# Performance work log

Hardware: AMD Instinct MI355X
Metric: run time of the kernel (lower is better)

Reference implementation:

```python
import jax, jax.numpy as jnp
import numpy as np

DIM = 2048
H = 16
KV_RANK = 512
NOPE = 128
ROPE_D = 64
VD = 128
QK = NOPE + ROPE_D  # 192
SCALE = QK ** -0.5
B, S = 2, 2048
EPS = 1e-5


def _rope(x, start_pos):
    # x: (b, s, h, d) or (b, s, d); rotate along last dim, positions along axis 1
    s = x.shape[1]
    d = x.shape[-1]
    half = d // 2
    inv_freq = 1.0 / (10000.0 ** (jnp.arange(half, dtype=jnp.float32) * (2.0 / d)))
    pos = jnp.arange(start_pos, start_pos + s, dtype=jnp.float32)
    ang = pos[:, None] * inv_freq[None, :]  # (s, half)
    cos, sin = jnp.cos(ang), jnp.sin(ang)
    if x.ndim == 4:
        cos, sin = cos[None, :, None, :], sin[None, :, None, :]
    else:
        cos, sin = cos[None, :, :], sin[None, :, :]
    x1, x2 = x[..., :half], x[..., half:]
    return jnp.concatenate([x1 * cos - x2 * sin, x2 * cos + x1 * sin], axis=-1).astype(x.dtype)


def _layernorm(x, w, b):
    mu = jnp.mean(x, axis=-1, keepdims=True)
    var = jnp.mean(jnp.square(x - mu), axis=-1, keepdims=True)
    return (x - mu) * jax.lax.rsqrt(var + EPS) * w + b


def setup_inputs() -> dict:
    key = jax.random.key(0)
    ks = jax.random.split(key, 6)
    std = 0.02
    x = jax.random.normal(ks[0], (B, S, DIM), dtype=jnp.float32)
    wq = jax.random.normal(ks[1], (H * QK, DIM), dtype=jnp.float32) * std
    wkv_a = jax.random.normal(ks[2], (KV_RANK + ROPE_D, DIM), dtype=jnp.float32) * std
    wkv_b = jax.random.normal(ks[3], (H * (NOPE + VD), KV_RANK), dtype=jnp.float32) * std
    wo = jax.random.normal(ks[4], (DIM, H * VD), dtype=jnp.float32) * std
    kv_norm_w = jnp.ones((KV_RANK,), dtype=jnp.float32)
    kv_norm_b = jnp.zeros((KV_RANK,), dtype=jnp.float32)
    return {"x": x, "wq": wq, "wkv_a": wkv_a, "kv_norm_w": kv_norm_w,
            "kv_norm_b": kv_norm_b, "wkv_b": wkv_b, "wo": wo, "start_pos": 0}


def reference(x, wq, wkv_a, kv_norm_w, kv_norm_b, wkv_b, wo, start_pos):
    b, s, _ = x.shape
    # query projection: (b,s,H,QK)
    q = (x @ wq.T).reshape(b, s, H, QK)
    q_nope, q_pe = q[..., :NOPE], q[..., NOPE:]
    q_pe = _rope(q_pe, start_pos)
    # compressed kv + rope key
    kv_all = x @ wkv_a.T                      # (b,s,KV_RANK+ROPE_D)
    kv, k_pe = kv_all[..., :KV_RANK], kv_all[..., KV_RANK:]
    k_pe = _rope(k_pe, start_pos)             # (b,s,ROPE_D)
    kvn = _layernorm(kv, kv_norm_w, kv_norm_b)  # (b,s,KV_RANK)
    # absorb path: expand compressed kv through per-head wkv_b blocks
    w = wkv_b.reshape(H, NOPE + VD, KV_RANK)
    k_nope = jnp.einsum('btc,hdc->bthd', kvn, w[:, :NOPE])   # (b,t,H,NOPE)
    v = jnp.einsum('btc,hdc->bthd', kvn, w[:, NOPE:])        # (b,t,H,VD)
    q_full = jnp.concatenate([q_nope, q_pe], axis=-1)        # (b,s,H,QK)
    k_full = jnp.concatenate(
        [k_nope, jnp.broadcast_to(k_pe[:, :, None, :], (b, s, H, ROPE_D))], axis=-1)
    scores = jnp.einsum('bshd,bthd->bhst', q_full, k_full) * SCALE
    causal = jnp.tril(jnp.ones((s, s), dtype=bool))
    scores = jnp.where(causal[None, None], scores, jnp.float32(-1e30))
    attn = jax.nn.softmax(scores, axis=-1)
    out = jnp.einsum('bhst,bthd->bshd', attn, v).reshape(b, s, H * VD)
    return out @ wo.T
```

## Files before the change

kernel.cpp:

```cpp
#include <hip/hip_runtime.h>
#include <hip/hip_bf16.h>
#include <math.h>

typedef __bf16 bf16_t;
typedef __bf16 bf16x2 __attribute__((ext_vector_type(2)));
typedef __bf16 bf16x4 __attribute__((ext_vector_type(4)));
typedef __bf16 bf16x8 __attribute__((ext_vector_type(8)));
typedef float f32x4 __attribute__((ext_vector_type(4)));

#define SEQ 2048
#define MLA_SCALE 0.07216878364870322f
#define LN_EPS 1e-5f

__device__ __forceinline__ void gload_lds16(const bf16_t* g, bf16_t* l) {
    __builtin_amdgcn_global_load_lds(
        (const __attribute__((address_space(1))) uint32_t*)(const void*)g,
        (__attribute__((address_space(3))) uint32_t*)(void*)l, 16, 0, 0);
}

__global__ __launch_bounds__(256)
void cvt_f32_bf16(const float* __restrict__ in, bf16_t* __restrict__ out, int n4) {
    for (int i = blockIdx.x * 256 + threadIdx.x; i < n4; i += gridDim.x * 256) {
        float4 v = ((const float4*)in)[i];
        bf16x4 p = { (bf16_t)v.x, (bf16_t)v.y, (bf16_t)v.z, (bf16_t)v.w };
        ((bf16x4*)out)[i] = p;
    }
}

#define G256_PHASE(TAU, KS, MH, HTO, MAT, WAITV)                               \
{                                                                              \
    const int slot_ = (2 * (TAU) + (KS)) & 3;                                  \
    bf16x8 af_[4];                                                             \
    {                                                                          \
        const bf16_t* ab_ = As + slot_ * 8192 +                                \
                            (wm2 * 128 + (MH) * 64 + lr) * 32 + rdcol;         \
        _Pragma("unroll")                                                      \
        for (int f = 0; f < 4; ++f) af_[f] = *(const bf16x8*)(ab_ + f * 512);  \
    }                                                                          \
    if ((MH) == 0) {                                                           \
        const bf16_t* bb_ = Bs + slot_ * 8192 + (wn2 * 64 + lr) * 32 + rdcol;  \
        _Pragma("unroll")                                                      \
        for (int f = 0; f < 4; ++f) bq[f] = *(const bf16x8*)(bb_ + f * 512);   \
    }                                                                          \
    if ((MAT) == 0) stageA(2 * T + 3 + (HTO)); else stageB(2 * T + 3 + (HTO)); \
    __builtin_amdgcn_s_barrier();                                              \
    asm volatile("" ::: "memory");                                             \
    __builtin_amdgcn_s_setprio(1);                                             \
    _Pragma("unroll")                                                          \
    for (int f = 0; f < 4; ++f)                                                \
        _Pragma("unroll")                                                      \
        for (int n = 0; n < 4; ++n)                                            \
            acc[(MH) * 4 + f][n] = __builtin_amdgcn_mfma_f32_16x16x32_bf16(    \
                af_[f], bq[n], acc[(MH) * 4 + f][n], 0, 0, 0);                 \
    __builtin_amdgcn_s_setprio(0);                                             \
    asm volatile("" ::: "memory");                                             \
    if (WAITV) asm volatile("s_waitcnt vmcnt(8)" ::: "memory");                \
    __builtin_amdgcn_s_barrier();                                              \
}

template<int MODE>
__global__ __launch_bounds__(512, 2)
void gemm256(const bf16_t* __restrict__ A, const bf16_t* __restrict__ B,
             float* __restrict__ C, bf16_t* __restrict__ out0,
             bf16_t* __restrict__ out1, int N, int K) {
    __shared__ __attribute__((aligned(16))) bf16_t As[32768];
    __shared__ __attribute__((aligned(16))) bf16_t Bs[32768];
    __shared__ __attribute__((aligned(16))) bf16_t Ds[8192];

    const int tid = threadIdx.x;
    const int lane = tid & 63, w = tid >> 6;
    const int lr = lane & 15, kh = lane >> 4;
    const int wm2 = w >> 2, wn2 = w & 3;
    const int bm = blockIdx.y, bn = blockIdx.x;
    const int NT = K >> 6;

    const int rdcol = 8 * (kh ^ ((lr >> 1) & 3));
    const int strow = (w << 5) + (lane >> 2);
    const int scol = 8 * ((lane & 3) ^ ((lane >> 3) & 3));

    f32x4 acc[8][4];
    #pragma unroll
    for (int i = 0; i < 8; ++i)
        #pragma unroll
        for (int j = 0; j < 4; ++j) acc[i][j] = 0.0f;

    auto stageA = [&](int ht) {
        int hs = (ht < 2 * NT) ? ht : (2 * NT - 1);
        int tau = hs >> 1, kap = hs & 1;
        const bf16_t* g = A + (size_t)(bm * 256 + strow) * K + tau * 64 + kap * 32 + scol;
        bf16_t* l = (ht < 2 * NT) ? (As + (ht & 3) * 8192 + w * 1024) : (Ds + w * 1024);
        gload_lds16(g, l);
        gload_lds16(g + (size_t)16 * K, l + 512);
    };
    auto stageB = [&](int ht) {
        int hs = (ht < 2 * NT) ? ht : (2 * NT - 1);
        int tau = hs >> 1, kap = hs & 1;
        const bf16_t* g = B + (size_t)(bn * 256 + strow) * K + tau * 64 + kap * 32 + scol;
        bf16_t* l = (ht < 2 * NT) ? (Bs + (ht & 3) * 8192 + w * 1024) : (Ds + w * 1024);
        gload_lds16(g, l);
        gload_lds16(g + (size_t)16 * K, l + 512);
    };

    stageA(0); stageB(0); stageA(1); stageB(1); stageA(2); stageB(2);
    asm volatile("s_waitcnt vmcnt(8)" ::: "memory");
    __builtin_amdgcn_s_barrier();

    for (int it = 0; it < (NT >> 1); ++it) {
        const int T = 2 * it;
        bf16x8 bq[4];
        G256_PHASE(T,     0, 0, 0, 0, 0)
        G256_PHASE(T,     0, 1, 0, 1, 1)
        G256_PHASE(T,     1, 0, 1, 0, 0)
        G256_PHASE(T,     1, 1, 1, 1, 1)
        G256_PHASE(T + 1, 0, 0, 2, 0, 0)
        G256_PHASE(T + 1, 0, 1, 2, 1, 1)
        G256_PHASE(T + 1, 1, 0, 3, 0, 0)
        G256_PHASE(T + 1, 1, 1, 3, 1, 1)
    }

    const int rg = kh * 4;
    if (MODE == 0) {
        #pragma unroll
        for (int mf = 0; mf < 8; ++mf)
            #pragma unroll
            for (int nf = 0; nf < 4; ++nf) {
                size_t row0 = (size_t)(bm * 256 + wm2 * 128 + mf * 16 + rg);
                int col = bn * 256 + wn2 * 64 + nf * 16 + lr;
                #pragma unroll
                for (int rr = 0; rr < 4; ++rr)
                    C[(row0 + rr) * N + col] = acc[mf][nf][rr];
            }
    } else if (MODE == 1) {
        const int h = bn;
        #pragma unroll
        for (int mf = 0; mf < 8; ++mf)
            #pragma unroll
            for (int nf = 0; nf < 4; ++nf) {
                int d = wn2 * 64 + nf * 16 + lr;
                int trow = bm * 256 + wm2 * 128 + mf * 16 + rg;
                int b = trow >> 11, t = trow & 2047;
                if (d < 128) {
                    bf16_t* p = out0 + ((size_t)(b * 16 + h) * SEQ + t) * 192 + d;
                    #pragma unroll
                    for (int rr = 0; rr < 4; ++rr)
                        p[rr * 192] = (bf16_t)acc[mf][nf][rr];
                } else {
                    bf16x4 pv = { (bf16_t)acc[mf][nf][0], (bf16_t)acc[mf][nf][1],
                                  (bf16_t)acc[mf][nf][2], (bf16_t)acc[mf][nf][3] };
                    *(bf16x4*)(out1 + ((size_t)(b * 16 + h) * 128 + (d - 128)) * SEQ + t) = pv;
                }
            }
    } else {
        #pragma unroll
        for (int mf = 0; mf < 8; ++mf)
            #pragma unroll
            for (int nf = 0; nf < 4; ++nf) {
                int n = bn * 256 + wn2 * 64 + nf * 16 + lr;
                int h = n / 192, d = n - h * 192;
                int trow = bm * 256 + wm2 * 128 + mf * 16 + rg;
                int b = trow >> 11, t = trow & 2047;
                bf16_t* p = out0 + ((size_t)(b * 16 + h) * SEQ + t) * 192 + d;
                #pragma unroll
                for (int rr = 0; rr < 4; ++rr)
                    p[rr * 192] = (bf16_t)acc[mf][nf][rr];
            }
    }
}

__device__ __forceinline__ void gemm_core(const bf16_t* __restrict__ A,
                                          const bf16_t* __restrict__ B,
                                          int N, int K, int bm, int bn,
                                          bf16_t* As, bf16_t* Bs,
                                          f32x4 (&acc)[4][4]) {
    const int tid = threadIdx.x;
    const int lane = tid & 63, w = tid >> 6;
    const int lr = lane & 15, kh = lane >> 4;
    const int wm = (w >> 1) * 64, wn = (w & 1) * 64;
    const int subrow = lane >> 2;
    const int colel = (lane & 3) * 8;

    const int rA = bm * 128 + 32 * w + subrow;
    const int rB = bn * 128 + 32 * w + subrow;
    const int rb1 = (rB < N) ? rB : (N - 1);
    const int rb2 = (rB + 16 < N) ? (rB + 16) : (N - 1);

    for (int kt = 0; kt < K; kt += 32) {
        __syncthreads();
        gload_lds16(A + (size_t)rA * K + kt + colel,        As + (2 * w) * 512);
        gload_lds16(A + (size_t)(rA + 16) * K + kt + colel, As + (2 * w + 1) * 512);
        gload_lds16(B + (size_t)rb1 * K + kt + colel,       Bs + (2 * w) * 512);
        gload_lds16(B + (size_t)rb2 * K + kt + colel,       Bs + (2 * w + 1) * 512);
        __syncthreads();
        bf16x8 af[4], bfr[4];
        #pragma unroll
        for (int im = 0; im < 4; ++im)
            af[im] = *(const bf16x8*)(As + (wm + im * 16 + lr) * 32 + kh * 8);
        #pragma unroll
        for (int jn = 0; jn < 4; ++jn)
            bfr[jn] = *(const bf16x8*)(Bs + (wn + jn * 16 + lr) * 32 + kh * 8);
        #pragma unroll
        for (int im = 0; im < 4; ++im)
            #pragma unroll
            for (int jn = 0; jn < 4; ++jn)
                acc[im][jn] = __builtin_amdgcn_mfma_f32_16x16x32_bf16(
                    af[im], bfr[jn], acc[im][jn], 0, 0, 0);
    }
}

__global__ __launch_bounds__(256)
void gemm_nt(const bf16_t* __restrict__ A, const bf16_t* __restrict__ B,
             float* __restrict__ C, int M, int N, int K) {
    __shared__ bf16_t As[4096], Bs[4096];
    f32x4 acc[4][4];
    #pragma unroll
    for (int i = 0; i < 4; ++i)
        #pragma unroll
        for (int j = 0; j < 4; ++j) acc[i][j] = 0.0f;
    gemm_core(A, B, N, K, blockIdx.y, blockIdx.x, As, Bs, acc);

    const int tid = threadIdx.x, lane = tid & 63, w = tid >> 6;
    const int lr = lane & 15, rg = (lane >> 4) * 4;
    const int wm = (w >> 1) * 64, wn = (w & 1) * 64;
    #pragma unroll
    for (int im = 0; im < 4; ++im)
        #pragma unroll
        for (int jn = 0; jn < 4; ++jn) {
            int col = blockIdx.x * 128 + wn + jn * 16 + lr;
            if (col >= N) continue;
            size_t rowb = (size_t)(blockIdx.y * 128 + wm + im * 16 + rg);
            #pragma unroll
            for (int rr = 0; rr < 4; ++rr)
                C[(rowb + rr) * N + col] = acc[im][jn][rr];
        }
}

__global__ __launch_bounds__(256)
void rope_ln(const float* __restrict__ kv_all,
             const float* __restrict__ lnw, const float* __restrict__ lnb,
             bf16_t* __restrict__ kvnb, bf16_t* __restrict__ kpack,
             float2* __restrict__ rope_cs, const int* __restrict__ start_pos) {
    const int m = blockIdx.x;
    const int tid = threadIdx.x;
    const int b = m >> 11, t = m & 2047;
    const float pos = (float)(start_pos[0] + t);
    __shared__ float red[8];
    __shared__ float stats[2];
    __shared__ float kbuf[64];

    const float* kvrow = kv_all + (size_t)m * 576;
    float v0 = kvrow[tid], v1 = kvrow[tid + 256];
    float ssum = v0 + v1, ssq = v0 * v0 + v1 * v1;
    for (int off = 32; off > 0; off >>= 1) {
        ssum += __shfl_down(ssum, off);
        ssq  += __shfl_down(ssq, off);
    }
    const int lane = tid & 63, wid = tid >> 6;
    if (lane == 0) { red[wid] = ssum; red[4 + wid] = ssq; }
    __syncthreads();
    if (tid == 0) {
        float ts = red[0] + red[1] + red[2] + red[3];
        float tq = red[4] + red[5] + red[6] + red[7];
        float mu = ts * (1.0f / 512.0f);
        float var = tq * (1.0f / 512.0f) - mu * mu;
        stats[0] = mu;
        stats[1] = rsqrtf(var + LN_EPS);
    }
    if (tid < 32) {
        int j = tid;
        float inv = expf(-(float)j * 0.2878231366242554f);
        float ang = pos * inv;
        float c = cosf(ang), sn = sinf(ang);
        float x1 = kvrow[512 + j], x2 = kvrow[544 + j];
        kbuf[j]      = x1 * c - x2 * sn;
        kbuf[32 + j] = x2 * c + x1 * sn;
        if (b == 0) rope_cs[t * 32 + j] = make_float2(c, sn);
    }
    __syncthreads();
    float mu = stats[0], rstd = stats[1];
    kvnb[(size_t)m * 512 + tid]       = (bf16_t)((v0 - mu) * rstd * lnw[tid] + lnb[tid]);
    kvnb[(size_t)m * 512 + tid + 256] = (bf16_t)((v1 - mu) * rstd * lnw[tid + 256] + lnb[tid + 256]);

    {
        int hh = tid >> 4, j4 = (tid & 15) * 4;
        bf16x4 pk = { (bf16_t)kbuf[j4], (bf16_t)kbuf[j4 + 1],
                      (bf16_t)kbuf[j4 + 2], (bf16_t)kbuf[j4 + 3] };
        *(bf16x4*)(kpack + ((size_t)(b * 16 + hh) * SEQ + t) * 192 + 128 + j4) = pk;
    }
}

__global__ __launch_bounds__(256, 2)
void attn_mfma(const bf16_t* __restrict__ qb, const bf16_t* __restrict__ kpack,
               const bf16_t* __restrict__ vt, const float2* __restrict__ rope_cs,
               bf16_t* __restrict__ ao) {
    __shared__ bf16_t Ks[64][200];
    __shared__ bf16_t Vts[128][72];
    __shared__ bf16_t Pls[4][16][72];

    const int bx = blockIdx.x, h = blockIdx.y, b = blockIdx.z;
    const int tid = threadIdx.x;
    const int lane = tid & 63, w = tid >> 6;
    const int lr = lane & 15, kh = lane >> 4;
    const size_t bS = (size_t)b * SEQ;
    const bf16_t* kbase = kpack + (size_t)(b * 16 + h) * SEQ * 192;
    const bf16_t* vbase = vt + (size_t)(b * 16 + h) * 128 * SEQ;

    int krow_[6], koff_[6], vd_[4], vt8_[4];
    #pragma unroll
    for (int i = 0; i < 6; ++i) { int c = tid + 256 * i; krow_[i] = c / 24; koff_[i] = (c % 24) * 8; }
    #pragma unroll
    for (int i = 0; i < 4; ++i) { int c = tid + 256 * i; vd_[i] = c >> 3; vt8_[i] = (c & 7) * 8; }

    for (int half = 0; half < 2; ++half) {
        const int qt = half ? bx : (31 - bx);
        const int q0 = qt * 64;
        const int myrow = q0 + w * 16;
        const int qabs = myrow + lr;

        bf16x8 qf[6];
        {
            const bf16_t* qrow = qb + ((size_t)(b * 16 + h) * SEQ + qabs) * 192;
            #pragma unroll
            for (int ks = 0; ks < 6; ++ks)
                qf[ks] = *(const bf16x8*)(qrow + ks * 32 + kh * 8);
            const float2* csp = rope_cs + (size_t)qabs * 32 + kh * 8;
            #pragma unroll
            for (int i = 0; i < 8; ++i) {
                float2 cs = csp[i];
                float x1 = (float)qf[4][i], x2 = (float)qf[5][i];
                qf[4][i] = (bf16_t)(x1 * cs.x - x2 * cs.y);
                qf[5][i] = (bf16_t)(x2 * cs.x + x1 * cs.y);
            }
        }

        f32x4 O[8];
        #pragma unroll
        for (int i = 0; i < 8; ++i) O[i] = 0.0f;
        float m_r = -1e30f, l_r = 0.0f;

        bf16x8 rk[6], rv[4];
        #pragma unroll
        for (int i = 0; i < 6; ++i)
            rk[i] = *(const bf16x8*)(kbase + (size_t)krow_[i] * 192 + koff_[i]);
        #pragma unroll
        for (int i = 0; i < 4; ++i)
            rv[i] = *(const bf16x8*)(vbase + (size_t)vd_[i] * SEQ + vt8_[i]);

        for (int kt = 0; kt <= qt; ++kt) {
            __syncthreads();
            #pragma unroll
            for (int i = 0; i < 6; ++i) *(bf16x8*)&Ks[krow_[i]][koff_[i]] = rk[i];
            #pragma unroll
            for (int i = 0; i < 4; ++i) *(bf16x8*)&Vts[vd_[i]][vt8_[i]] = rv[i];
            if (kt < qt) {
                const int t1 = (kt + 1) * 64;
                #pragma unroll
                for (int i = 0; i < 6; ++i)
                    rk[i] = *(const bf16x8*)(kbase + (size_t)(t1 + krow_[i]) * 192 + koff_[i]);
                #pragma unroll
                for (int i = 0; i < 4; ++i)
                    rv[i] = *(const bf16x8*)(vbase + (size_t)vd_[i] * SEQ + t1 + vt8_[i]);
            }
            __syncthreads();

            f32x4 sacc[4];
            #pragma unroll
            for (int j = 0; j < 4; ++j) sacc[j] = 0.0f;
            __builtin_amdgcn_s_setprio(1);
            #pragma unroll
            for (int ks = 0; ks < 6; ++ks)
                #pragma unroll
                for (int j = 0; j < 4; ++j) {
                    bf16x8 kf = *(const bf16x8*)&Ks[j * 16 + lr][ks * 32 + kh * 8];
                    sacc[j] = __builtin_amdgcn_mfma_f32_16x16x32_bf16(kf, qf[ks], sacc[j], 0, 0, 0);
                }
            __builtin_amdgcn_s_setprio(0);

            const int t0 = kt * 64;
            float p[16];
            if (kt == qt) {
                #pragma unroll
                for (int j = 0; j < 4; ++j)
                    #pragma unroll
                    for (int rr = 0; rr < 4; ++rr) {
                        int tabs = t0 + j * 16 + kh * 4 + rr;
                        p[j * 4 + rr] = (tabs > qabs) ? -1e30f : sacc[j][rr] * MLA_SCALE;
                    }
            } else {
                #pragma unroll
                for (int j = 0; j < 4; ++j)
                    #pragma unroll
                    for (int rr = 0; rr < 4; ++rr)
                        p[j * 4 + rr] = sacc[j][rr] * MLA_SCALE;
            }

            float mx = p[0];
            #pragma unroll
            for (int e = 1; e < 16; ++e) mx = fmaxf(mx, p[e]);
            mx = fmaxf(mx, __shfl_xor(mx, 16));
            mx = fmaxf(mx, __shfl_xor(mx, 32));
            float mnew = fmaxf(m_r, mx);
            float cr = __expf(m_r - mnew);
            float ps = 0.0f;
            #pragma unroll
            for (int e = 0; e < 16; ++e) {
                p[e] = __expf(p[e] - mnew);
                ps += p[e];
            }
            ps += __shfl_xor(ps, 16);
            ps += __shfl_xor(ps, 32);
            l_r = l_r * cr + ps;
            m_r = mnew;

            float corr[4];
            #pragma unroll
            for (int rr = 0; rr < 4; ++rr)
                corr[rr] = __shfl(cr, kh * 4 + rr);
            #pragma unroll
            for (int dt = 0; dt < 8; ++dt)
                #pragma unroll
                for (int rr = 0; rr < 4; ++rr)
                    O[dt][rr] *= corr[rr];

            #pragma unroll
            for (int j = 0; j < 4; ++j)
                #pragma unroll
                for (int rr2 = 0; rr2 < 2; ++rr2) {
                    bf16x2 pp = { (bf16_t)p[j * 4 + 2 * rr2], (bf16_t)p[j * 4 + 2 * rr2 + 1] };
                    *(bf16x2*)&Pls[w][lr][j * 16 + kh * 4 + 2 * rr2] = pp;
                }
            bf16x8 pa0 = *(const bf16x8*)&Pls[w][lr][kh * 8];
            bf16x8 pa1 = *(const bf16x8*)&Pls[w][lr][32 + kh * 8];
            __builtin_amdgcn_s_setprio(1);
            #pragma unroll
            for (int dt = 0; dt < 8; ++dt) {
                bf16x8 b0 = *(const bf16x8*)&Vts[dt * 16 + lr][kh * 8];
                O[dt] = __builtin_amdgcn_mfma_f32_16x16x32_bf16(pa0, b0, O[dt], 0, 0, 0);
                bf16x8 b1 = *(const bf16x8*)&Vts[dt * 16 + lr][32 + kh * 8];
                O[dt] = __builtin_amdgcn_mfma_f32_16x16x32_bf16(pa1, b1, O[dt], 0, 0, 0);
            }
            __builtin_amdgcn_s_setprio(0);
        }

        float linv[4];
        #pragma unroll
        for (int rr = 0; rr < 4; ++rr)
            linv[rr] = 1.0f / __shfl(l_r, kh * 4 + rr);
        #pragma unroll
        for (int rr = 0; rr < 4; ++rr) {
            size_t rowb = (bS + myrow + kh * 4 + rr) * 2048 + h * 128;
            #pragma unroll
            for (int dt = 0; dt < 8; ++dt)
                ao[rowb + dt * 16 + lr] = (bf16_t)(O[dt][rr] * linv[rr]);
        }
    }
}

extern "C" void kernel_launch(void* const* d_in, const int* in_sizes, int n_in,
                              void* d_out, int out_size, void* d_ws, size_t ws_size,
                              hipStream_t stream) {
    const float* x     = (const float*)d_in[0];
    const float* wq    = (const float*)d_in[1];
    const float* wkv_a = (const float*)d_in[2];
    const float* lnw   = (const float*)d_in[3];
    const float* lnb   = (const float*)d_in[4];
    const float* wkv_b = (const float*)d_in[5];
    const float* wo    = (const float*)d_in[6];
    const int* start_pos = (const int*)d_in[7];
    float* out = (float*)d_out;

    char* w8 = (char*)d_ws;
    bf16_t* xb   = (bf16_t*)(w8);
    bf16_t* wqb  = (bf16_t*)(w8 + 16777216);
    bf16_t* wab  = (bf16_t*)(w8 + 29360128);
    bf16_t* wbb  = (bf16_t*)(w8 + 31719424);
    bf16_t* wob  = (bf16_t*)(w8 + 35913728);
    bf16_t* kvnb = (bf16_t*)(w8 + 44302336);
    bf16_t* kpk  = (bf16_t*)(w8 + 48496640);
    bf16_t* vtb  = (bf16_t*)(w8 + 73662464);
    bf16_t* aob  = (bf16_t*)(w8 + 90439680);
    bf16_t* qbh  = (bf16_t*)(w8 + 107216896);
    float*  kva  = (float*)(w8 + 132382720);
    float2* rcs  = (float2*)(w8 + 141819904);

    cvt_f32_bf16<<<2048, 256, 0, stream>>>(x,     xb,  8388608 / 4);
    cvt_f32_bf16<<<2048, 256, 0, stream>>>(wq,    wqb, 6291456 / 4);
    cvt_f32_bf16<<<1152, 256, 0, stream>>>(wkv_a, wab, 1179648 / 4);
    cvt_f32_bf16<<<2048, 256, 0, stream>>>(wkv_b, wbb, 2097152 / 4);
    cvt_f32_bf16<<<2048, 256, 0, stream>>>(wo,    wob, 4194304 / 4);

    gemm256<2><<<dim3(12, 16), 512, 0, stream>>>(xb, wqb, nullptr, qbh, nullptr, 3072, 2048);
    gemm_nt<<<dim3(5, 32), 256, 0, stream>>>(xb, wab, kva, 4096, 576, 2048);
    rope_ln<<<4096, 256, 0, stream>>>(kva, lnw, lnb, kvnb, kpk, rcs, start_pos);
    gemm256<1><<<dim3(16, 16), 512, 0, stream>>>(kvnb, wbb, nullptr, kpk, vtb, 4096, 512);
    attn_mfma<<<dim3(16, 16, 2), 256, 0, stream>>>(qbh, kpk, vtb, rcs, aob);
    gemm_nt<<<dim3(16, 32), 256, 0, stream>>>(aob, wob, out, 4096, 2048, 2048);
}
```

Baseline: 308.5 us.

## Remap blocks to XCDs for L2 locality and add lazy softmax rescaling

```diff
diff --git a/kernel.cpp b/kernel.cpp
--- a/kernel.cpp
+++ b/kernel.cpp
@@ -16,6 +16,16 @@
     __builtin_amdgcn_global_load_lds(
         (const __attribute__((address_space(1))) uint32_t*)(const void*)g,
         (__attribute__((address_space(3))) uint32_t*)(void*)l, 16, 0, 0);
+}
+
+__device__ __forceinline__ void xcd_map(int bid, int total, int nbn,
+                                        int& bm, int& bn) {
+    int per = total >> 3;
+    int cbm = per / nbn;
+    int xcd = bid & 7, s = bid >> 3;
+    int q = s / nbn;
+    bm = xcd * cbm + q;
+    bn = s - q * nbn;
 }
 
 __global__ __launch_bounds__(256)
@@ -62,7 +72,7 @@
 __global__ __launch_bounds__(512, 2)
 void gemm256(const bf16_t* __restrict__ A, const bf16_t* __restrict__ B,
              float* __restrict__ C, bf16_t* __restrict__ out0,
-             bf16_t* __restrict__ out1, int N, int K) {
+             bf16_t* __restrict__ out1, int N, int K, int total, int nbn) {
     __shared__ __attribute__((aligned(16))) bf16_t As[32768];
     __shared__ __attribute__((aligned(16))) bf16_t Bs[32768];
     __shared__ __attribute__((aligned(16))) bf16_t Ds[8192];
@@ -71,7 +81,8 @@
     const int lane = tid & 63, w = tid >> 6;
     const int lr = lane & 15, kh = lane >> 4;
     const int wm2 = w >> 2, wn2 = w & 3;
-    const int bm = blockIdx.y, bn = blockIdx.x;
+    int bm, bn;
+    xcd_map(blockIdx.x, total, nbn, bm, bn);
     const int NT = K >> 6;
 
     const int rdcol = 8 * (kh ^ ((lr >> 1) & 3));
@@ -167,17 +178,25 @@
     }
 }
 
-__device__ __forceinline__ void gemm_core(const bf16_t* __restrict__ A,
-                                          const bf16_t* __restrict__ B,
-                                          int N, int K, int bm, int bn,
-                                          bf16_t* As, bf16_t* Bs,
-                                          f32x4 (&acc)[4][4]) {
+__global__ __launch_bounds__(256)
+void gemm_nt(const bf16_t* __restrict__ A, const bf16_t* __restrict__ B,
+             float* __restrict__ C, int M, int N, int K, int total, int nbn) {
+    __shared__ bf16_t As[4096], Bs[4096];
+    int bm, bn;
+    xcd_map(blockIdx.x, total, nbn, bm, bn);
+
     const int tid = threadIdx.x;
     const int lane = tid & 63, w = tid >> 6;
     const int lr = lane & 15, kh = lane >> 4;
     const int wm = (w >> 1) * 64, wn = (w & 1) * 64;
     const int subrow = lane >> 2;
     const int colel = (lane & 3) * 8;
+
+    f32x4 acc[4][4];
+    #pragma unroll
+    for (int i = 0; i < 4; ++i)
+        #pragma unroll
+        for (int j = 0; j < 4; ++j) acc[i][j] = 0.0f;
 
     const int rA = bm * 128 + 32 * w + subrow;
     const int rB = bn * 128 + 32 * w + subrow;
@@ -205,29 +224,15 @@
                 acc[im][jn] = __builtin_amdgcn_mfma_f32_16x16x32_bf16(
                     af[im], bfr[jn], acc[im][jn], 0, 0, 0);
     }
-}
-
-__global__ __launch_bounds__(256)
-void gemm_nt(const bf16_t* __restrict__ A, const bf16_t* __restrict__ B,
-             float* __restrict__ C, int M, int N, int K) {
-    __shared__ bf16_t As[4096], Bs[4096];
-    f32x4 acc[4][4];
-    #pragma unroll
-    for (int i = 0; i < 4; ++i)
-        #pragma unroll
-        for (int j = 0; j < 4; ++j) acc[i][j] = 0.0f;
-    gemm_core(A, B, N, K, blockIdx.y, blockIdx.x, As, Bs, acc);
-
-    const int tid = threadIdx.x, lane = tid & 63, w = tid >> 6;
-    const int lr = lane & 15, rg = (lane >> 4) * 4;
-    const int wm = (w >> 1) * 64, wn = (w & 1) * 64;
+
+    const int rg = kh * 4;
     #pragma unroll
     for (int im = 0; im < 4; ++im)
         #pragma unroll
         for (int jn = 0; jn < 4; ++jn) {
-            int col = blockIdx.x * 128 + wn + jn * 16 + lr;
+            int col = bn * 128 + wn + jn * 16 + lr;
             if (col >= N) continue;
-            size_t rowb = (size_t)(blockIdx.y * 128 + wm + im * 16 + rg);
+            size_t rowb = (size_t)(bm * 128 + wm + im * 16 + rg);
             #pragma unroll
             for (int rr = 0; rr < 4; ++rr)
                 C[(rowb + rr) * N + col] = acc[im][jn][rr];
@@ -296,7 +301,12 @@
     __shared__ bf16_t Vts[128][72];
     __shared__ bf16_t Pls[4][16][72];
 
-    const int bx = blockIdx.x, h = blockIdx.y, b = blockIdx.z;
+    const int bid = blockIdx.x;
+    const int xcd = bid & 7, s = bid >> 3;
+    const int g = xcd * 4 + (s >> 4);
+    const int bx = s & 15;
+    const int h = g & 15, b = g >> 4;
+
     const int tid = threadIdx.x;
     const int lane = tid & 63, w = tid >> 6;
     const int lr = lane & 15, kh = lane >> 4;
@@ -398,36 +408,39 @@
             for (int e = 1; e < 16; ++e) mx = fmaxf(mx, p[e]);
             mx = fmaxf(mx, __shfl_xor(mx, 16));
             mx = fmaxf(mx, __shfl_xor(mx, 32));
-            float mnew = fmaxf(m_r, mx);
-            float cr = __expf(m_r - mnew);
+
+            if (!__all(mx <= m_r + 8.0f)) {
+                float mnew = fmaxf(m_r, mx);
+                float cr = __expf(m_r - mnew);
+                l_r *= cr;
+                m_r = mnew;
+                float corr[4];
+                #pragma unroll
+                for (int rr = 0; rr < 4; ++rr)
+                    corr[rr] = __shfl(cr, kh * 4 + rr);
+                #pragma unroll
+                for (int dt = 0; dt < 8; ++dt)
+                    #pragma unroll
+                    for (int rr = 0; rr < 4; ++rr)
+                        O[dt][rr] *= corr[rr];
+            }
+
             float ps = 0.0f;
             #pragma unroll
             for (int e = 0; e < 16; ++e) {
-                p[e] = __expf(p[e] - mnew);
+                p[e] = __expf(p[e] - m_r);
                 ps += p[e];
             }
             ps += __shfl_xor(ps, 16);
             ps += __shfl_xor(ps, 32);
-            l_r = l_r * cr + ps;
-            m_r = mnew;
-
-            float corr[4];
-            #pragma unroll
-            for (int rr = 0; rr < 4; ++rr)
-                corr[rr] = __shfl(cr, kh * 4 + rr);
-            #pragma unroll
-            for (int dt = 0; dt < 8; ++dt)
-                #pragma unroll
-                for (int rr = 0; rr < 4; ++rr)
-                    O[dt][rr] *= corr[rr];
-
-            #pragma unroll
-            for (int j = 0; j < 4; ++j)
-                #pragma unroll
-                for (int rr2 = 0; rr2 < 2; ++rr2) {
-                    bf16x2 pp = { (bf16_t)p[j * 4 + 2 * rr2], (bf16_t)p[j * 4 + 2 * rr2 + 1] };
-                    *(bf16x2*)&Pls[w][lr][j * 16 + kh * 4 + 2 * rr2] = pp;
-                }
+            l_r += ps;
+
+            #pragma unroll
+            for (int j = 0; j < 4; ++j) {
+                bf16x4 pp = { (bf16_t)p[j * 4], (bf16_t)p[j * 4 + 1],
+                              (bf16_t)p[j * 4 + 2], (bf16_t)p[j * 4 + 3] };
+                *(bf16x4*)&Pls[w][lr][j * 16 + kh * 4] = pp;
+            }
             bf16x8 pa0 = *(const bf16x8*)&Pls[w][lr][kh * 8];
             bf16x8 pa1 = *(const bf16x8*)&Pls[w][lr][32 + kh * 8];
             __builtin_amdgcn_s_setprio(1);
@@ -488,10 +501,10 @@
     cvt_f32_bf16<<<2048, 256, 0, stream>>>(wkv_b, wbb, 2097152 / 4);
     cvt_f32_bf16<<<2048, 256, 0, stream>>>(wo,    wob, 4194304 / 4);
 
-    gemm256<2><<<dim3(12, 16), 512, 0, stream>>>(xb, wqb, nullptr, qbh, nullptr, 3072, 2048);
-    gemm_nt<<<dim3(5, 32), 256, 0, stream>>>(xb, wab, kva, 4096, 576, 2048);
+    gemm256<2><<<192, 512, 0, stream>>>(xb, wqb, nullptr, qbh, nullptr, 3072, 2048, 192, 12);
+    gemm_nt<<<160, 256, 0, stream>>>(xb, wab, kva, 4096, 576, 2048, 160, 5);
     rope_ln<<<4096, 256, 0, stream>>>(kva, lnw, lnb, kvnb, kpk, rcs, start_pos);
-    gemm256<1><<<dim3(16, 16), 512, 0, stream>>>(kvnb, wbb, nullptr, kpk, vtb, 4096, 512);
-    attn_mfma<<<dim3(16, 16, 2), 256, 0, stream>>>(qbh, kpk, vtb, rcs, aob);
-    gemm_nt<<<dim3(16, 32), 256, 0, stream>>>(aob, wob, out, 4096, 2048, 2048);
-}
+    gemm256<1><<<256, 512, 0, stream>>>(kvnb, wbb, nullptr, kpk, vtb, 4096, 512, 256, 16);
+    attn_mfma<<<512, 256, 0, stream>>>(qbh, kpk, vtb, rcs, aob);
+    gemm_nt<<<512, 256, 0, stream>>>(aob, wob, out, 4096, 2048, 2048, 512, 16);
+}
```

After: 287.6 us. 1.07x faster.
